# Kernel tuning notes

Hardware: AMD Instinct MI355X
Metric: run time of the kernel (lower is better)

## Reference

```python
import jax, jax.numpy as jnp
import numpy as np

R = 32  # voxel resolution
B, CIN, COUT, N = 4, 64, 64, 4096
K = 3


def setup_inputs():
    key = jax.random.key(0)
    ks = jax.random.split(key, 8)
    s = 0.05
    return {
        "features": jax.random.normal(ks[0], (B, CIN, N), jnp.float32),
        "coords": jax.random.normal(ks[1], (B, 3, N), jnp.float32),
        # voxel branch: conv3d + BN x2
        "w1": jax.random.normal(ks[2], (COUT, CIN, K, K, K), jnp.float32) * s,
        "b1": jnp.zeros((COUT,), jnp.float32),
        "g1": jnp.ones((COUT,), jnp.float32),
        "be1": jnp.zeros((COUT,), jnp.float32),
        "w2": jax.random.normal(ks[3], (COUT, COUT, K, K, K), jnp.float32) * s,
        "b2": jnp.zeros((COUT,), jnp.float32),
        "g2": jnp.ones((COUT,), jnp.float32),
        "be2": jnp.zeros((COUT,), jnp.float32),
        # point branch SharedMLP (1x1 conv + BN + ReLU)
        "wp": jax.random.normal(ks[4], (COUT, CIN), jnp.float32) * s,
        "bp": jnp.zeros((COUT,), jnp.float32),
        "gp": jnp.ones((COUT,), jnp.float32),
        "bep": jnp.zeros((COUT,), jnp.float32),
        # fuzzy_proj 1x1 conv
        "wf": jax.random.normal(ks[5], (COUT, CIN), jnp.float32) * s,
        "bf": jnp.zeros((COUT,), jnp.float32),
        # fusion SharedMLP (3*COUT -> COUT)
        "wfu": jax.random.normal(ks[6], (COUT, 3 * COUT), jnp.float32) * s,
        "bfu": jnp.zeros((COUT,), jnp.float32),
        "gfu": jnp.ones((COUT,), jnp.float32),
        "befu": jnp.zeros((COUT,), jnp.float32),
    }


def _bn3d(x, g, b):
    # training-mode BatchNorm3d, eps=1e-4 (biased variance, as torch)
    m = x.mean((0, 2, 3, 4), keepdims=True)
    v = x.var((0, 2, 3, 4), keepdims=True)
    return (x - m) * jax.lax.rsqrt(v + 1e-4) * g[None, :, None, None, None] + b[None, :, None, None, None]


def _bn1d(x, g, b):
    m = x.mean((0, 2), keepdims=True)
    v = x.var((0, 2), keepdims=True)
    return (x - m) * jax.lax.rsqrt(v + 1e-4) * g[None, :, None] + b[None, :, None]


def _conv3d(x, w, b):
    pad = K // 2
    y = jax.lax.conv_general_dilated(x, w, (1, 1, 1), [(pad, pad)] * 3,
                                     dimension_numbers=('NCDHW', 'OIDHW', 'NCDHW'))
    return y + b[None, :, None, None, None]


def _conv1x1(x, w, b):
    return jnp.einsum('oc,bcn->bon', w, x) + b[None, :, None]


def _voxelize(features, coords):
    # PVCNN Voxelization(normalize=True, eps=0): center, scale to unit, grid coords in [0, R-1]
    nc = coords - coords.mean(axis=2, keepdims=True)              # [B,3,N]
    norm = jnp.linalg.norm(nc, axis=1, keepdims=True)             # [B,1,N]
    nc = nc / (norm.max(axis=2, keepdims=True) * 2.0) + 0.5
    nc = jnp.clip(nc * R, 0.0, R - 1)
    vox = jnp.round(nc).astype(jnp.int32)                         # [B,3,N]
    b_, c_, n_ = features.shape
    idx = (vox[:, 0] * R + vox[:, 1]) * R + vox[:, 2]             # [B,N]
    flat = (idx + jnp.arange(b_)[:, None] * R ** 3).reshape(-1)
    feat = features.transpose(0, 2, 1).reshape(b_ * n_, c_)
    sums = jax.ops.segment_sum(feat, flat, num_segments=b_ * R ** 3)
    cnt = jax.ops.segment_sum(jnp.ones((b_ * n_,), feat.dtype), flat, num_segments=b_ * R ** 3)
    avg = sums / jnp.maximum(cnt, 1.0)[:, None]                   # scatter-mean
    grid = avg.reshape(b_, R ** 3, c_).transpose(0, 2, 1).reshape(b_, c_, R, R, R)
    return grid, nc


def _devoxelize(grid, nc):
    # trilinear gather: grid [B,C,R,R,R], nc [B,3,N] float coords in [0,R-1]
    b_, c_ = grid.shape[:2]
    g = grid.reshape(b_, c_, -1)
    lo_f = jnp.floor(nc)
    fr = nc - lo_f                                                # fractional part [B,3,N]
    lo = lo_f.astype(jnp.int32)
    hi = jnp.minimum(lo + 1, R - 1)
    out = jnp.zeros((b_, c_, nc.shape[2]), grid.dtype)
    for dx in (0, 1):
        for dy in (0, 1):
            for dz in (0, 1):
                ix = hi[:, 0] if dx else lo[:, 0]
                iy = hi[:, 1] if dy else lo[:, 1]
                iz = hi[:, 2] if dz else lo[:, 2]
                w = ((fr[:, 0] if dx else 1.0 - fr[:, 0]) *
                     (fr[:, 1] if dy else 1.0 - fr[:, 1]) *
                     (fr[:, 2] if dz else 1.0 - fr[:, 2]))        # [B,N]
                flat = (ix * R + iy) * R + iz                     # [B,N]
                vals = jnp.take_along_axis(g, flat[:, None, :], axis=2)  # [B,C,N]
                out = out + vals * w[:, None, :]
    return out


def reference(features, coords, w1, b1, g1, be1, w2, b2, g2, be2,
              wp, bp, gp, bep, wf, bf, wfu, bfu, gfu, befu):
    lrelu = lambda x: jnp.where(x > 0, x, 0.1 * x)
    # voxel branch
    grid, nc = _voxelize(features, coords)
    v = lrelu(_bn3d(_conv3d(grid, w1, b1), g1, be1))
    v = lrelu(_bn3d(_conv3d(v, w2, b2), g2, be2))
    vox_feat = _devoxelize(v, nc)                                 # [B,COUT,N]
    # point branch
    pt = jax.nn.relu(_bn1d(_conv1x1(features, wp, bp), gp, bep))
    # fuzzy branch: dense attention over points
    cn = coords.transpose(0, 2, 1)                                # [B,N,3]
    cn = cn / jnp.maximum(jnp.linalg.norm(cn, axis=-1, keepdims=True), 1e-12)
    att = jax.nn.softmax(jnp.einsum('bnd,bmd->bnm', cn, cn) / 0.1, axis=-1)
    fz = jnp.einsum('bnm,bcm->bcn', att, features)                # [B,CIN,N]
    fz = _conv1x1(fz, wf, bf)
    # fusion
    comb = jnp.concatenate([vox_feat, pt, fz], axis=1)            # [B,3*COUT,N]
    fused = jax.nn.relu(_bn1d(_conv1x1(comb, wfu, bfu), gfu, befu))
    return (fused, coords)
```

## Files before the change

kernel.cpp:

```cpp
#include <hip/hip_runtime.h>
#include <hip/hip_bf16.h>
#include <math.h>

#define RR 32
#define R3 32768
#define BB 4
#define CI 64
#define CO 64
#define NN 4096

typedef short v8s __attribute__((ext_vector_type(8)));
typedef float v4f __attribute__((ext_vector_type(4)));
typedef unsigned short ushort_t;

__device__ __forceinline__ unsigned short f2bf(float f) {
    unsigned int u = __float_as_uint(f);
    unsigned int r = (u + 0x7FFFu + ((u >> 16) & 1u)) >> 16;
    return (unsigned short)r;
}
__device__ __forceinline__ float bf2f(unsigned short h) {
    return __uint_as_float((unsigned int)h << 16);
}

__device__ __forceinline__ void gll16(const void* g, void* l) {
    __builtin_amdgcn_global_load_lds((const __attribute__((address_space(1))) unsigned int*)g,
                                     (__attribute__((address_space(3))) unsigned int*)l, 16, 0, 0);
}

__device__ __forceinline__ float blockReduceSum(float v, float* sm) {
    int tid = threadIdx.x;
    sm[tid] = v; __syncthreads();
    for (int off = 128; off > 0; off >>= 1) {
        if (tid < off) sm[tid] += sm[tid + off];
        __syncthreads();
    }
    float r = sm[0]; __syncthreads();
    return r;
}
__device__ __forceinline__ float blockReduceMax(float v, float* sm) {
    int tid = threadIdx.x;
    sm[tid] = v; __syncthreads();
    for (int off = 128; off > 0; off >>= 1) {
        if (tid < off) sm[tid] = fmaxf(sm[tid], sm[tid + off]);
        __syncthreads();
    }
    float r = sm[0]; __syncthreads();
    return r;
}

__global__ void k_nc(const float* __restrict__ coords, float* __restrict__ nc,
                     int* __restrict__ vidx, int* __restrict__ cntI) {
    int b = blockIdx.x, tid = threadIdx.x;
    __shared__ float sm[256];
    const float* cb = coords + (size_t)b * 3 * NN;
    float s0 = 0, s1 = 0, s2 = 0;
    for (int n = tid; n < NN; n += 256) {
        s0 += cb[n]; s1 += cb[NN + n]; s2 += cb[2 * NN + n];
    }
    float m0 = blockReduceSum(s0, sm) * (1.0f / NN);
    float m1 = blockReduceSum(s1, sm) * (1.0f / NN);
    float m2 = blockReduceSum(s2, sm) * (1.0f / NN);
    float mx = 0;
    for (int n = tid; n < NN; n += 256) {
        float dx = cb[n] - m0, dy = cb[NN + n] - m1, dz = cb[2 * NN + n] - m2;
        mx = fmaxf(mx, dx * dx + dy * dy + dz * dz);
    }
    mx = blockReduceMax(mx, sm);
    float denom = 2.0f * sqrtf(mx);
    float mean[3] = {m0, m1, m2};
    for (int n = tid; n < NN; n += 256) {
        int vi[3];
        #pragma unroll
        for (int ax = 0; ax < 3; ax++) {
            float x = (cb[ax * NN + n] - mean[ax]) / denom + 0.5f;
            x = x * RR;
            x = fminf(fmaxf(x, 0.0f), (float)(RR - 1));
            nc[((size_t)b * 3 + ax) * NN + n] = x;
            vi[ax] = (int)rintf(x);
        }
        int idx = (vi[0] * RR + vi[1]) * RR + vi[2];
        vidx[b * NN + n] = idx;
        atomicAdd(&cntI[b * R3 + idx], 1);
    }
}

__global__ void k_scan1(const int* __restrict__ cntI, int* __restrict__ lscan,
                        int* __restrict__ bsum) {
    __shared__ int sm[256];
    int tid = threadIdx.x;
    int i = blockIdx.x * 256 + tid;
    int v = cntI[i];
    sm[tid] = v; __syncthreads();
    for (int off = 1; off < 256; off <<= 1) {
        int t = (tid >= off) ? sm[tid - off] : 0;
        __syncthreads();
        sm[tid] += t;
        __syncthreads();
    }
    lscan[i] = sm[tid] - v;
    if (tid == 255) bsum[blockIdx.x] = sm[tid];
}

__global__ void k_scan2(const int* __restrict__ bsum, int* __restrict__ bbase) {
    __shared__ int sm[512];
    int tid = threadIdx.x;
    int v = bsum[tid];
    sm[tid] = v; __syncthreads();
    for (int off = 1; off < 512; off <<= 1) {
        int t = (tid >= off) ? sm[tid - off] : 0;
        __syncthreads();
        sm[tid] += t;
        __syncthreads();
    }
    bbase[tid] = sm[tid] - v;
}

__global__ void k_fill(const int* __restrict__ vidx, const int* __restrict__ lscan,
                       const int* __restrict__ bbase, int* __restrict__ rank,
                       int* __restrict__ plist) {
    int i = blockIdx.x * 256 + threadIdx.x;
    int b = i >> 12, n = i & (NN - 1);
    int flat = b * R3 + vidx[i];
    int r = atomicAdd(&rank[flat], 1);
    plist[bbase[flat >> 8] + lscan[flat] + r] = n;
}

__global__ void k_pfeat(const float* __restrict__ feat, float* __restrict__ featT,
                        ushort_t* __restrict__ featb) {
    __shared__ float t[64][65];
    int b = blockIdx.y, n0 = blockIdx.x * 64, tid = threadIdx.x;
    int q = tid >> 6, nl = tid & 63;
    #pragma unroll
    for (int k = 0; k < 16; k++) {
        int c = q * 16 + k;
        float v = feat[((size_t)(b * CI + c)) * NN + n0 + nl];
        t[nl][c] = v;
        featb[((size_t)(b * CI + c)) * NN + n0 + nl] = f2bf(v);
    }
    __syncthreads();
    #pragma unroll
    for (int k = 0; k < 16; k++) {
        int n = q * 16 + k;
        featT[((size_t)b * NN + n0 + n) * 64 + nl] = t[n][nl];
    }
}

__global__ __launch_bounds__(256) void k_gather(const float* __restrict__ featT,
                                                const int* __restrict__ cntI,
                                                const int* __restrict__ lscan,
                                                const int* __restrict__ bbase,
                                                const int* __restrict__ plist,
                                                ushort_t* __restrict__ gT) {
    int wv = threadIdx.x >> 6, lane = threadIdx.x & 63;
    int vbase = blockIdx.x * 32 + wv * 8;
    for (int k = 0; k < 8; k++) {
        int flat = vbase + k;
        int count = cntI[flat];
        float s = 0.0f;
        if (count > 0) {
            int b = flat >> 15;
            int start = bbase[flat >> 8] + lscan[flat];
            for (int j = 0; j < count; j++) {
                int n = plist[start + j];
                s += featT[((size_t)b * NN + n) * 64 + lane];
            }
            s *= 1.0f / (float)count;
        }
        gT[(size_t)flat * 64 + lane] = f2bf(s);
    }
}

__global__ void k_tws(const float* __restrict__ w1, const float* __restrict__ w2,
                      ushort_t* __restrict__ wS1, ushort_t* __restrict__ wS2) {
    int i = blockIdx.x * 256 + threadIdx.x;
    const float* w = (i < 110592) ? w1 : w2;
    ushort_t* wS = (i < 110592) ? wS1 : wS2;
    int j = (i < 110592) ? i : i - 110592;
    int cis = j & 31, co = (j >> 5) & 63;
    int dx = (j >> 11) % 3, cih = (j / 6144) & 1, dzdy = j / 12288;
    int k = dzdy * 3 + dx, ci = cih * 32 + cis;
    wS[j] = f2bf(w[((size_t)co * CI + ci) * 27 + k]);
}

__global__ void k_fold(const float* __restrict__ wp, const float* __restrict__ wfu,
                       const float* __restrict__ wf, const float* __restrict__ bf,
                       const float* __restrict__ bfu,
                       float* __restrict__ wpT, float* __restrict__ wfuT,
                       float* __restrict__ bC, float* __restrict__ accs) {
    int i = blockIdx.x * 256 + threadIdx.x;
    if (i < 4096) {
        int c = i >> 6, o = i & 63;
        wpT[c * 64 + o] = wp[o * 64 + c];
    } else if (i < 12288) {
        int j = i - 4096;
        int c = j >> 6, o = j & 63;
        wfuT[c * 64 + o] = wfu[(size_t)o * 192 + c];
    } else if (i < 16384) {
        int j = i - 12288;
        int c = j >> 6, o = j & 63;
        float s = 0;
        for (int k = 0; k < 64; k++)
            s += wfu[(size_t)o * 192 + 128 + k] * wf[(size_t)k * 64 + c];
        wfuT[(128 + c) * 64 + o] = s;
    } else if (i < 16448) {
        int o = i - 16384;
        float s = bfu[o];
        for (int k = 0; k < 64; k++)
            s += wfu[(size_t)o * 192 + 128 + k] * bf[k];
        bC[o] = s;
    } else if (i < 16960) {
        accs[i - 16448] = 0.0f;
    }
}

__global__ void k_bncast2(const ushort_t* __restrict__ x, const float* __restrict__ accs,
                          const float* __restrict__ g, const float* __restrict__ be,
                          float invcnt, float slope, ushort_t* __restrict__ o) {
    size_t i = (size_t)blockIdx.x * 256 + threadIdx.x;
    int c0 = (int)((i * 8) & 63);
    float sc[8], sh[8];
    #pragma unroll
    for (int j = 0; j < 8; j++) {
        int c = c0 + j;
        float mean = accs[2 * c] * invcnt;
        float var = accs[2 * c + 1] * invcnt - mean * mean;
        float scale = g[c] * rsqrtf(var + 1e-4f);
        sc[j] = scale;
        sh[j] = be[c] - mean * scale;
    }
    uint4 in = ((const uint4*)x)[i];
    unsigned iv[4] = {in.x, in.y, in.z, in.w};
    unsigned pk[4];
    #pragma unroll
    for (int j = 0; j < 4; j++) {
        float u0 = bf2f((unsigned short)(iv[j] & 0xFFFF)) * sc[2 * j] + sh[2 * j];
        float u1 = bf2f((unsigned short)(iv[j] >> 16)) * sc[2 * j + 1] + sh[2 * j + 1];
        u0 = u0 > 0 ? u0 : slope * u0;
        u1 = u1 > 0 ? u1 : slope * u1;
        pk[j] = (unsigned)f2bf(u0) | ((unsigned)f2bf(u1) << 16);
    }
    ((uint4*)o)[i] = make_uint4(pk[0], pk[1], pk[2], pk[3]);
}

template <int OUTBF16>
__global__ __launch_bounds__(256) void k_convlds(const ushort_t* __restrict__ gT,
                                                 const ushort_t* __restrict__ wS,
                                                 void* __restrict__ outP,
                                                 float* __restrict__ accs) {
    __shared__ ushort_t lin[20480];
    __shared__ ushort_t lw[2][6144];
    int bid = blockIdx.x;
    int wgid = (bid & 7) * 64 + (bid >> 3);
    int yt = wgid & 3, z0 = (wgid >> 2) & 31, b = wgid >> 7;
    int tid = threadIdx.x;
    int w = __builtin_amdgcn_readfirstlane(tid >> 6);
    int lane = tid & 63, l15 = lane & 15, l4 = lane >> 4;
    int y0 = yt * 8;
    const ushort_t* gTb = gT + (size_t)b * R3 * 64;

    int voxF[4];
    #pragma unroll
    for (int f = 0; f < 4; f++)
        voxF[f] = (w * 2 + (f >> 1)) * 32 + (f & 1) * 16 + l15 - 1;
    bool xlo_ok = (l15 != 0), xhi_ok = (l15 != 15);

    int lsw = lane ^ ((lane >> 3) & 7);
    int wsz8 = ((l15 * 4 + l4) ^ ((l15 >> 1) & 7)) * 8;

    const v8s vzero = {};
    v4f acc[4][4];
    #pragma unroll
    for (int m = 0; m < 4; m++)
        #pragma unroll
        for (int f = 0; f < 4; f++)
            acc[m][f] = (v4f){0.0f, 0.0f, 0.0f, 0.0f};

#define WSTAGE(s)                                                              \
    do {                                                                       \
        const ushort_t* _src = wS + (size_t)(s) * 6144;                        \
        ushort_t* _dst = lw[(s) & 1];                                          \
        _Pragma("unroll") for (int _i = 0; _i < 3; _i++) {                     \
            int _pb = _i * 256 + w * 64;                                       \
            gll16(_src + (size_t)(_pb + lsw) * 8, _dst + (size_t)(_pb + lane) * 8); \
        }                                                                      \
    } while (0)

#define ISTAGE(dz)                                                             \
    do {                                                                       \
        int _zp = z0 - 1 + (dz);                                               \
        if (_zp < 0 || _zp > 31) {                                             \
            for (int _q = 0; _q < 10; _q++)                                    \
                *(v8s*)&lin[(size_t)(w * 640 + _q * 64 + lane) * 8] = vzero;   \
        } else {                                                               \
            if (yt == 0) *(v8s*)&lin[(size_t)tid * 8] = vzero;                 \
            if (yt == 3) *(v8s*)&lin[(size_t)(2304 + tid) * 8] = vzero;        \
            const ushort_t* _pb = gTb + ((size_t)_zp * 1024 + (size_t)(y0 - 1) * 32) * 64; \
            int _g0 = (yt == 0) ? 256 : 0;                                     \
            int _nc = 10 - (yt == 0) - (yt == 3);                              \
            for (int _i = 0; _i < _nc; _i++) {                                 \
                int _pbase = _g0 + _i * 256 + w * 64;                          \
                int _p = _pbase + lane;                                        \
                int _vx = _p >> 3, _js = _p & 7;                               \
                int _sg = _vx * 8 + (_js ^ (_vx & 7));                         \
                gll16(_pb + (size_t)_sg * 8, lin + (size_t)_pbase * 8);        \
            }                                                                  \
        }                                                                      \
    } while (0)

    WSTAGE(0);
    for (int s = 0; s < 18; s++) {
        int dy = (s / 2) % 3, cih = s & 1;
        asm volatile("s_barrier" ::: "memory");
        if ((s % 6) == 0) ISTAGE(s / 6);
        if (s + 1 < 18) WSTAGE(s + 1);
        if (s + 1 < 18) asm volatile("s_waitcnt vmcnt(3) lgkmcnt(0)" ::: "memory");
        else            asm volatile("s_waitcnt vmcnt(0) lgkmcnt(0)" ::: "memory");
        asm volatile("s_barrier" ::: "memory");

        const ushort_t* lwb = lw[s & 1];
        #pragma unroll
        for (int dx = 0; dx < 3; dx++) {
            v8s Bf[4];
            #pragma unroll
            for (int f = 0; f < 4; f++) {
                int vox = voxF[f] + dy * 32 + dx;
                int g = vox * 8 + ((cih * 4 + l4) ^ (vox & 7));
                int bix = g * 16;
                bix = bix < 0 ? 0 : bix;
                v8s vb = *(const v8s*)((const char*)lin + bix);
                bool ok = (dx == 0 && (f & 1) == 0) ? xlo_ok :
                          (dx == 2 && (f & 1) == 1) ? xhi_ok : true;
                Bf[f] = ok ? vb : vzero;
            }
            const ushort_t* ap = lwb + dx * 2048 + wsz8;
            #pragma unroll
            for (int m = 0; m < 4; m++) {
                v8s Af = *(const v8s*)(ap + m * 512);
                #pragma unroll
                for (int f = 0; f < 4; f++)
                    acc[m][f] = __builtin_amdgcn_mfma_f32_16x16x32_bf16(Af, Bf[f], acc[m][f], 0, 0, 0);
            }
        }
    }

    #pragma unroll
    for (int m = 0; m < 4; m++) {
        #pragma unroll
        for (int f = 0; f < 4; f++) {
            int y = y0 + w * 2 + (f >> 1);
            int x = (f & 1) * 16 + l15;
            size_t base = ((size_t)b * R3 + z0 * 1024 + y * 32 + x) * 64 + m * 16 + l4 * 4;
            if (OUTBF16) {
                unsigned p0 = (unsigned)f2bf(acc[m][f][0]) | ((unsigned)f2bf(acc[m][f][1]) << 16);
                unsigned p1 = (unsigned)f2bf(acc[m][f][2]) | ((unsigned)f2bf(acc[m][f][3]) << 16);
                *(uint2*)&((ushort_t*)outP)[base] = make_uint2(p0, p1);
            } else {
                float4 o = make_float4(acc[m][f][0], acc[m][f][1], acc[m][f][2], acc[m][f][3]);
                *(float4*)&((float*)outP)[base] = o;
            }
        }
    }

    __syncthreads();
    float* sbuf = (float*)lin;
    #pragma unroll
    for (int m = 0; m < 4; m++)
        #pragma unroll
        for (int r = 0; r < 4; r++) {
            float s = 0, q = 0;
            #pragma unroll
            for (int f = 0; f < 4; f++) {
                float v = acc[m][f][r];
                s += v; q += v * v;
            }
            sbuf[tid * 33 + (m * 4 + r) * 2] = s;
            sbuf[tid * 33 + (m * 4 + r) * 2 + 1] = q;
        }
    __syncthreads();
    if (tid < 128) {
        int co = tid >> 1, val = tid & 1;
        int m = co >> 4, cl4 = (co >> 2) & 3, r = co & 3;
        float a = 0;
        for (int w2 = 0; w2 < 4; w2++)
            for (int l = 0; l < 16; l++)
                a += sbuf[(w2 * 64 + cl4 * 16 + l) * 33 + (m * 4 + r) * 2 + val];
        atomicAdd(&accs[2 * co + val], a);
    }
#undef WSTAGE
#undef ISTAGE
}

__global__ void k_bnfin2(const float* __restrict__ pst, const float* __restrict__ g,
                         const float* __restrict__ be, float* __restrict__ stats,
                         float invcnt) {
    int c = blockIdx.x, tid = threadIdx.x;
    __shared__ float rs[256], rq[256];
    rs[tid] = pst[(c * 256 + tid) * 2];
    rq[tid] = pst[(c * 256 + tid) * 2 + 1];
    __syncthreads();
    for (int off = 128; off > 0; off >>= 1) {
        if (tid < off) { rs[tid] += rs[tid + off]; rq[tid] += rq[tid + off]; }
        __syncthreads();
    }
    if (tid == 0) {
        float mean = rs[0] * invcnt;
        float var = rq[0] * invcnt - mean * mean;
        float sc = g[c] * rsqrtf(var + 1e-4f);
        stats[2 * c] = sc;
        stats[2 * c + 1] = be[c] - mean * sc;
    }
}

__global__ void k_bn_act(const float* __restrict__ x, const float* __restrict__ stats,
                         float* __restrict__ out, int shift, float slope) {
    size_t i = (size_t)blockIdx.x * 256 + threadIdx.x;
    int c = (int)((i >> shift) & 63);
    float sc = stats[2 * c], sh = stats[2 * c + 1];
    float4 v = ((const float4*)x)[i];
    v.x = v.x * sc + sh; v.y = v.y * sc + sh; v.z = v.z * sc + sh; v.w = v.w * sc + sh;
    v.x = v.x > 0 ? v.x : slope * v.x;
    v.y = v.y > 0 ? v.y : slope * v.y;
    v.z = v.z > 0 ? v.z : slope * v.z;
    v.w = v.w > 0 ? v.w : slope * v.w;
    ((float4*)out)[i] = v;
}

__global__ void k_devox2(const ushort_t* __restrict__ gcl, const float* __restrict__ accs,
                         const float* __restrict__ g, const float* __restrict__ be,
                         float invcnt, const float* __restrict__ nc,
                         float* __restrict__ out) {
    int b = blockIdx.y;
    int tid = threadIdx.x, p = tid >> 4, q = tid & 15;
    int n = blockIdx.x * 16 + p;
    float x = nc[((size_t)b * 3 + 0) * NN + n];
    float y = nc[((size_t)b * 3 + 1) * NN + n];
    float z = nc[((size_t)b * 3 + 2) * NN + n];
    float fx = floorf(x), fy = floorf(y), fz = floorf(z);
    int lx = (int)fx, ly = (int)fy, lz = (int)fz;
    int hx = min(lx + 1, RR - 1), hy = min(ly + 1, RR - 1), hz = min(lz + 1, RR - 1);
    float frx = x - fx, fry = y - fy, frz = z - fz;
    int xx[2] = {lx, hx}, yy[2] = {ly, hy}, zz[2] = {lz, hz};
    float wx[2] = {1.0f - frx, frx}, wy[2] = {1.0f - fry, fry}, wz[2] = {1.0f - frz, frz};
    float sc[4], sh[4];
    #pragma unroll
    for (int j = 0; j < 4; j++) {
        int c = q * 4 + j;
        float mean = accs[2 * c] * invcnt;
        float var = accs[2 * c + 1] * invcnt - mean * mean;
        float scale = g[c] * rsqrtf(var + 1e-4f);
        sc[j] = scale;
        sh[j] = be[c] - mean * scale;
    }
    float a0 = 0, a1 = 0, a2 = 0, a3 = 0;
    #pragma unroll
    for (int dx = 0; dx < 2; dx++)
        #pragma unroll
        for (int dy = 0; dy < 2; dy++)
            #pragma unroll
            for (int dz = 0; dz < 2; dz++) {
                int idx = (xx[dx] * RR + yy[dy]) * RR + zz[dz];
                float wt = wx[dx] * wy[dy] * wz[dz];
                uint2 pv = *(const uint2*)&gcl[((size_t)b * R3 + idx) * 64 + q * 4];
                float v0 = bf2f((unsigned short)(pv.x & 0xFFFF));
                float v1 = bf2f((unsigned short)(pv.x >> 16));
                float v2 = bf2f((unsigned short)(pv.y & 0xFFFF));
                float v3 = bf2f((unsigned short)(pv.y >> 16));
                float u0 = v0 * sc[0] + sh[0]; u0 = u0 > 0 ? u0 : 0.1f * u0;
                float u1 = v1 * sc[1] + sh[1]; u1 = u1 > 0 ? u1 : 0.1f * u1;
                float u2 = v2 * sc[2] + sh[2]; u2 = u2 > 0 ? u2 : 0.1f * u2;
                float u3 = v3 * sc[3] + sh[3]; u3 = u3 > 0 ? u3 : 0.1f * u3;
                a0 += wt * u0; a1 += wt * u1; a2 += wt * u2; a3 += wt * u3;
            }
    out[((size_t)(b * 64 + q * 4 + 0)) * NN + n] = a0;
    out[((size_t)(b * 64 + q * 4 + 1)) * NN + n] = a1;
    out[((size_t)(b * 64 + q * 4 + 2)) * NN + n] = a2;
    out[((size_t)(b * 64 + q * 4 + 3)) * NN + n] = a3;
}

__global__ __launch_bounds__(256) void k_fuzzym(const float* __restrict__ coords,
                                                const ushort_t* __restrict__ featb,
                                                float* __restrict__ pnum,
                                                float* __restrict__ pden) {
    __shared__ float cm[3][1024];
    __shared__ ushort_t la[4][2048];
    int b = blockIdx.z, mc = blockIdx.y, nt = blockIdx.x;
    int tid = threadIdx.x;
    int w = tid >> 6, lane = tid & 63, l15 = lane & 15, l4 = lane >> 4;
    int m0 = mc * 1024;

    for (int i = tid; i < 1024; i += 256) {
        float a0 = coords[((size_t)b * 3 + 0) * NN + m0 + i];
        float a1 = coords[((size_t)b * 3 + 1) * NN + m0 + i];
        float a2 = coords[((size_t)b * 3 + 2) * NN + m0 + i];
        float inv = 1.0f / fmaxf(sqrtf(a0 * a0 + a1 * a1 + a2 * a2), 1e-12f);
        cm[0][i] = a0 * inv; cm[1][i] = a1 * inv; cm[2][i] = a2 * inv;
    }

    int n = nt * 64 + w * 16 + l15;
    float q0 = coords[((size_t)b * 3 + 0) * NN + n];
    float q1 = coords[((size_t)b * 3 + 1) * NN + n];
    float q2 = coords[((size_t)b * 3 + 2) * NN + n];
    float qi = 10.0f / fmaxf(sqrtf(q0 * q0 + q1 * q1 + q2 * q2), 1e-12f);
    q0 *= qi; q1 *= qi; q2 *= qi;

    int srow = tid >> 2, sslot = tid & 3;
    int g0 = sslot ^ ((srow >> 1) & 3);
    const ushort_t* fb = featb + (size_t)b * 64 * NN + m0;
    const ushort_t* sbase = fb + (size_t)srow * NN + g0 * 8;
    int rsw = (l15 >> 1) & 3;

    v4f acc[4];
    #pragma unroll
    for (int cb = 0; cb < 4; cb++) acc[cb] = (v4f){0.0f, 0.0f, 0.0f, 0.0f};
    float den = 0.0f;

    gll16(sbase, &la[0][(size_t)tid * 8]);
    gll16(sbase + 32, &la[1][(size_t)tid * 8]);
    gll16(sbase + 64, &la[2][(size_t)tid * 8]);
    __syncthreads();

    for (int t = 0; t < 32; t++) {
        int cur = t & 3;
        asm volatile("s_waitcnt vmcnt(2)" ::: "memory");
        __syncthreads();
        if (t + 3 < 32)
            gll16(sbase + (t + 3) * 32, &la[(t + 3) & 3][(size_t)tid * 8]);

        int mo = t * 32 + l4 * 8;
        float e[8];
        #pragma unroll
        for (int jj = 0; jj < 2; jj++) {
            float4 x0 = *(const float4*)&cm[0][mo + jj * 4];
            float4 x1 = *(const float4*)&cm[1][mo + jj * 4];
            float4 x2 = *(const float4*)&cm[2][mo + jj * 4];
            e[jj * 4 + 0] = __expf(q0 * x0.x + q1 * x1.x + q2 * x2.x);
            e[jj * 4 + 1] = __expf(q0 * x0.y + q1 * x1.y + q2 * x2.y);
            e[jj * 4 + 2] = __expf(q0 * x0.z + q1 * x1.z + q2 * x2.z);
            e[jj * 4 + 3] = __expf(q0 * x0.w + q1 * x1.w + q2 * x2.w);
        }
        den += ((e[0] + e[1]) + (e[2] + e[3])) + ((e[4] + e[5]) + (e[6] + e[7]));
        union { __hip_bfloat162 h[4]; v8s v; } pk;
        pk.h[0] = __float22bfloat162_rn(make_float2(e[0], e[1]));
        pk.h[1] = __float22bfloat162_rn(make_float2(e[2], e[3]));
        pk.h[2] = __float22bfloat162_rn(make_float2(e[4], e[5]));
        pk.h[3] = __float22bfloat162_rn(make_float2(e[6], e[7]));
        #pragma unroll
        for (int cb = 0; cb < 4; cb++) {
            v8s A = *(const v8s*)&la[cur][(size_t)((cb * 16 + l15) * 4 + (l4 ^ rsw)) * 8];
            acc[cb] = __builtin_amdgcn_mfma_f32_16x16x32_bf16(A, pk.v, acc[cb], 0, 0, 0);
        }
        __syncthreads();
    }

    den += __shfl_xor(den, 16);
    den += __shfl_xor(den, 32);

    size_t obase = ((size_t)(b * 4 + mc)) * 64 * NN;
    #pragma unroll
    for (int cb = 0; cb < 4; cb++)
        #pragma unroll
        for (int r = 0; r < 4; r++)
            pnum[obase + (size_t)(cb * 16 + l4 * 4 + r) * NN + n] = acc[cb][r];
    if (l4 == 0) pden[((size_t)(b * 4 + mc)) * NN + n] = den;
}

__global__ void k_combine2(const float* __restrict__ pnum, const float* __restrict__ pden,
                           float* __restrict__ fzf) {
    int i = blockIdx.x * 256 + threadIdx.x;
    int b = i >> 18, c = (i >> 12) & 63, n = i & 4095;
    float num = 0, den = 0;
    #pragma unroll
    for (int ch = 0; ch < 4; ch++) {
        num += pnum[((size_t)(b * 4 + ch) * 64 + c) * NN + n];
        den += pden[((size_t)(b * 4 + ch)) * NN + n];
    }
    fzf[((size_t)(b * 64 + c)) * NN + n] = num / den;
}

__global__ __launch_bounds__(256) void k_1x1s(const float* __restrict__ in,
                                              const float* __restrict__ wT,
                                              const float* __restrict__ bias,
                                              float* __restrict__ out,
                                              float* __restrict__ pst) {
    int b = blockIdx.z, ob = blockIdx.y, bx = blockIdx.x;
    int tid = threadIdx.x;
    int q = tid & 15, o = ob * 16 + (tid >> 4);
    int n = bx * 64 + q * 4;
    const float* src = in + (size_t)b * 64 * NN + n;
    const float* wp_ = wT + o;
    v4f acc = {0, 0, 0, 0};
    #pragma unroll 8
    for (int c = 0; c < 64; c++) {
        float4 x = *(const float4*)&src[(size_t)c * NN];
        float w = wp_[c * 64];
        acc[0] += x.x * w; acc[1] += x.y * w; acc[2] += x.z * w; acc[3] += x.w * w;
    }
    float bv = bias[o];
    float s = 0, q2 = 0;
    float4 ov;
    float* op = (float*)&ov;
    #pragma unroll
    for (int v = 0; v < 4; v++) {
        float val = acc[v] + bv;
        op[v] = val;
        s += val; q2 += val * val;
    }
    *(float4*)&out[((size_t)(b * 64 + o)) * NN + n] = ov;
    #pragma unroll
    for (int off = 1; off < 16; off <<= 1) {
        s += __shfl_xor(s, off);
        q2 += __shfl_xor(q2, off);
    }
    if (q == 0) {
        int part = bx * 4 + b;
        pst[(o * 256 + part) * 2] = s;
        pst[(o * 256 + part) * 2 + 1] = q2;
    }
}

__global__ __launch_bounds__(256) void k_1x1f(const float* __restrict__ vox,
                                              const float* __restrict__ pt,
                                              const float* __restrict__ fzf,
                                              const float* __restrict__ bnB,
                                              const float* __restrict__ wfuT,
                                              const float* __restrict__ bC,
                                              float* __restrict__ out,
                                              float* __restrict__ pst) {
    int b = blockIdx.z, ob = blockIdx.y, bx = blockIdx.x;
    int tid = threadIdx.x;
    int q = tid & 15, o = ob * 16 + (tid >> 4);
    int n = bx * 64 + q * 4;
    const float* srcA = vox + (size_t)b * 64 * NN + n;
    const float* srcB = pt + (size_t)b * 64 * NN + n;
    const float* srcC = fzf + (size_t)b * 64 * NN + n;
    const float* wA = wfuT + o;
    v4f acc = {0, 0, 0, 0};
    #pragma unroll 8
    for (int c = 0; c < 64; c++) {
        float4 x = *(const float4*)&srcA[(size_t)c * NN];
        float w = wA[c * 64];
        acc[0] += x.x * w; acc[1] += x.y * w; acc[2] += x.z * w; acc[3] += x.w * w;
    }
    #pragma unroll 8
    for (int c = 0; c < 64; c++) {
        float4 x = *(const float4*)&srcB[(size_t)c * NN];
        float sc = bnB[2 * c], sh = bnB[2 * c + 1];
        float w = wA[(64 + c) * 64];
        float x0 = fmaxf(x.x * sc + sh, 0.0f), x1 = fmaxf(x.y * sc + sh, 0.0f);
        float x2 = fmaxf(x.z * sc + sh, 0.0f), x3 = fmaxf(x.w * sc + sh, 0.0f);
        acc[0] += x0 * w; acc[1] += x1 * w; acc[2] += x2 * w; acc[3] += x3 * w;
    }
    #pragma unroll 8
    for (int c = 0; c < 64; c++) {
        float4 x = *(const float4*)&srcC[(size_t)c * NN];
        float w = wA[(128 + c) * 64];
        acc[0] += x.x * w; acc[1] += x.y * w; acc[2] += x.z * w; acc[3] += x.w * w;
    }
    float bv = bC[o];
    float s = 0, q2 = 0;
    float4 ov;
    float* op = (float*)&ov;
    #pragma unroll
    for (int v = 0; v < 4; v++) {
        float val = acc[v] + bv;
        op[v] = val;
        s += val; q2 += val * val;
    }
    *(float4*)&out[((size_t)(b * 64 + o)) * NN + n] = ov;
    #pragma unroll
    for (int off = 1; off < 16; off <<= 1) {
        s += __shfl_xor(s, off);
        q2 += __shfl_xor(q2, off);
    }
    if (q == 0) {
        int part = bx * 4 + b;
        pst[(o * 256 + part) * 2] = s;
        pst[(o * 256 + part) * 2 + 1] = q2;
    }
}

extern "C" void kernel_launch(void* const* d_in, const int* in_sizes, int n_in,
                              void* d_out, int out_size, void* d_ws, size_t ws_size,
                              hipStream_t stream) {
    const float* features = (const float*)d_in[0];
    const float* coords = (const float*)d_in[1];
    const float* w1 = (const float*)d_in[2];
    const float* g1 = (const float*)d_in[4];
    const float* be1 = (const float*)d_in[5];
    const float* w2 = (const float*)d_in[6];
    const float* g2 = (const float*)d_in[8];
    const float* be2 = (const float*)d_in[9];
    const float* wp = (const float*)d_in[10];
    const float* bp = (const float*)d_in[11];
    const float* gp = (const float*)d_in[12];
    const float* bep = (const float*)d_in[13];
    const float* wf = (const float*)d_in[14];
    const float* bf = (const float*)d_in[15];
    const float* wfu = (const float*)d_in[16];
    const float* bfu = (const float*)d_in[17];
    const float* gfu = (const float*)d_in[18];
    const float* befu = (const float*)d_in[19];

    float* ws = (float*)d_ws;
    float* nc = ws;
    int* vidx = (int*)(ws + 49152);
    int* cntI = (int*)(ws + 65536);
    float* pden = ws + 65536;
    float* gridCL = ws + 196608;
    ushort_t* gTraw = (ushort_t*)gridCL;
    int* rank = (int*)(ws + 196608);
    int* lscan = (int*)(ws + 327680);
    int* bsum = (int*)(ws + 458752);
    int* bbase = (int*)(ws + 459264);
    int* plist = (int*)(ws + 459776);
    float* featT = ws + 476160;
    float* gTpool = ws + 8585216;
    ushort_t* gT = (ushort_t*)gTpool;
    float* pnum = gTpool;
    float* pstB = gTpool + 4194304;
    float* stats = ws + 16973824;
    float* voxreg = ws + 16974336;
    ushort_t* wS1 = (ushort_t*)voxreg;
    ushort_t* wS2 = wS1 + 110592;
    float* vox = voxreg;
    float* pt = ws + 18022912;
    float* fzf = ws + 19071488;
    float* wpT = ws + 20120064;
    float* wfuT = wpT + 4096;
    float* bC = wfuT + 12288;
    float* fpre = ws + 21168640;
    ushort_t* featb = (ushort_t*)fpre;
    float* accs = ws + 22217216;

    float* out = (float*)d_out;

    hipMemsetAsync(cntI, 0, (size_t)131072 * 4, stream);
    hipMemsetAsync(rank, 0, (size_t)131072 * 4, stream);

    k_fold<<<67, 256, 0, stream>>>(wp, wfu, wf, bf, bfu, wpT, wfuT, bC, accs);
    k_pfeat<<<dim3(64, BB), 256, 0, stream>>>(features, featT, featb);
    k_tws<<<864, 256, 0, stream>>>(w1, w2, wS1, wS2);

    k_nc<<<BB, 256, 0, stream>>>(coords, nc, vidx, cntI);
    k_scan1<<<512, 256, 0, stream>>>(cntI, lscan, bsum);
    k_scan2<<<1, 512, 0, stream>>>(bsum, bbase);
    k_fill<<<BB * NN / 256, 256, 0, stream>>>(vidx, lscan, bbase, rank, plist);
    k_gather<<<4096, 256, 0, stream>>>(featT, cntI, lscan, bbase, plist, gT);

    k_convlds<1><<<512, 256, 0, stream>>>(gT, wS1, gTraw, accs);
    k_bncast2<<<BB * R3 * 64 / 8 / 256, 256, 0, stream>>>(gTraw, accs, g1, be1,
                                                          1.0f / (BB * R3), 0.1f, gT);
    k_convlds<1><<<512, 256, 0, stream>>>(gT, wS2, gTraw, accs + 128);
    k_devox2<<<dim3(NN / 16, BB), 256, 0, stream>>>(gTraw, accs + 128, g2, be2,
                                                    1.0f / (BB * R3), nc, vox);

    k_fuzzym<<<dim3(64, 4, BB), 256, 0, stream>>>(coords, featb, pnum, pden);
    k_combine2<<<BB * 64 * NN / 256, 256, 0, stream>>>(pnum, pden, fzf);

    k_1x1s<<<dim3(NN / 64, 4, BB), 256, 0, stream>>>(features, wpT, bp, pt, pstB);
    k_bnfin2<<<64, 256, 0, stream>>>(pstB, gp, bep, stats + 256, 1.0f / (BB * NN));

    k_1x1f<<<dim3(NN / 64, 4, BB), 256, 0, stream>>>(vox, pt, fzf, stats + 256, wfuT, bC,
                                                     fpre, pstB);
    k_bnfin2<<<64, 256, 0, stream>>>(pstB, gfu, befu, stats + 384, 1.0f / (BB * NN));
    k_bn_act<<<BB * 64 * NN / 4 / 256, 256, 0, stream>>>(fpre, stats + 384, out, 10, 0.0f);

    hipMemcpyAsync(out + (size_t)BB * CO * NN, coords, (size_t)BB * 3 * NN * 4,
                   hipMemcpyDeviceToDevice, stream);
}
```

Before: 269.5 us.

## Merge prep kernels, fold memsets and BN finalize, drop fuzzy-loop barriers

Three preprocessing kernels (weight fold, weight swizzle, feature transpose) and the cntI memset become one block-indexed k_prep launch. The rank memset moves into k_scan1, and the final BN-statistics kernel is merged into the BN+ReLU kernel, which redoes the per-channel reduction in every block. The combine kernel is vectorised to float4. The __syncthreads in the k_fuzzym LDS pipeline are removed. The aim is fewer launches and less fixed per-kernel overhead, but dropping those barriers risks LDS races in the multi-buffered loop.

```diff
diff --git a/kernel.cpp b/kernel.cpp
--- a/kernel.cpp
+++ b/kernel.cpp
@@ -46,6 +46,74 @@
     }
     float r = sm[0]; __syncthreads();
     return r;
+}
+
+__global__ void k_prep(const float* __restrict__ wp, const float* __restrict__ wfu,
+                       const float* __restrict__ wf, const float* __restrict__ bf,
+                       const float* __restrict__ bfu,
+                       float* __restrict__ wpT, float* __restrict__ wfuT,
+                       float* __restrict__ bC, float* __restrict__ accs,
+                       const float* __restrict__ w1, const float* __restrict__ w2,
+                       ushort_t* __restrict__ wS1, ushort_t* __restrict__ wS2,
+                       const float* __restrict__ feat, float* __restrict__ featT,
+                       ushort_t* __restrict__ featb, int* __restrict__ cntI) {
+    __shared__ float t[64][65];
+    int bid = blockIdx.x, tid = threadIdx.x;
+    if (bid < 67) {
+        int i = bid * 256 + tid;
+        if (i < 4096) {
+            int c = i >> 6, o = i & 63;
+            wpT[c * 64 + o] = wp[o * 64 + c];
+        } else if (i < 12288) {
+            int j = i - 4096;
+            int c = j >> 6, o = j & 63;
+            wfuT[c * 64 + o] = wfu[(size_t)o * 192 + c];
+        } else if (i < 16384) {
+            int j = i - 12288;
+            int c = j >> 6, o = j & 63;
+            float s = 0;
+            for (int k = 0; k < 64; k++)
+                s += wfu[(size_t)o * 192 + 128 + k] * wf[(size_t)k * 64 + c];
+            wfuT[(128 + c) * 64 + o] = s;
+        } else if (i < 16448) {
+            int o = i - 16384;
+            float s = bfu[o];
+            for (int k = 0; k < 64; k++)
+                s += wfu[(size_t)o * 192 + 128 + k] * bf[k];
+            bC[o] = s;
+        } else if (i < 16960) {
+            accs[i - 16448] = 0.0f;
+        }
+    } else if (bid < 931) {
+        int i = (bid - 67) * 256 + tid;
+        const float* w = (i < 110592) ? w1 : w2;
+        ushort_t* wS = (i < 110592) ? wS1 : wS2;
+        int j = (i < 110592) ? i : i - 110592;
+        int cis = j & 31, co = (j >> 5) & 63;
+        int dx = (j >> 11) % 3, cih = (j / 6144) & 1, dzdy = j / 12288;
+        int k = dzdy * 3 + dx, ci = cih * 32 + cis;
+        wS[j] = f2bf(w[((size_t)co * CI + ci) * 27 + k]);
+    } else if (bid < 1187) {
+        int pb = bid - 931;
+        int b = pb >> 6, n0 = (pb & 63) * 64;
+        int q = tid >> 6, nl = tid & 63;
+        #pragma unroll
+        for (int k = 0; k < 16; k++) {
+            int c = q * 16 + k;
+            float v = feat[((size_t)(b * CI + c)) * NN + n0 + nl];
+            t[nl][c] = v;
+            featb[((size_t)(b * CI + c)) * NN + n0 + nl] = f2bf(v);
+        }
+        __syncthreads();
+        #pragma unroll
+        for (int k = 0; k < 16; k++) {
+            int n = q * 16 + k;
+            featT[((size_t)b * NN + n0 + n) * 64 + nl] = t[n][nl];
+        }
+    } else {
+        int z = (bid - 1187) * 256 + tid;
+        cntI[z] = 0;
+    }
 }
 
 __global__ void k_nc(const float* __restrict__ coords, float* __restrict__ nc,
@@ -85,10 +153,11 @@
 }
 
 __global__ void k_scan1(const int* __restrict__ cntI, int* __restrict__ lscan,
-                        int* __restrict__ bsum) {
+                        int* __restrict__ bsum, int* __restrict__ rank) {
     __shared__ int sm[256];
     int tid = threadIdx.x;
     int i = blockIdx.x * 256 + tid;
+    rank[i] = 0;
     int v = cntI[i];
     sm[tid] = v; __syncthreads();
     for (int off = 1; off < 256; off <<= 1) {
@@ -123,26 +192,6 @@
     int flat = b * R3 + vidx[i];
     int r = atomicAdd(&rank[flat], 1);
     plist[bbase[flat >> 8] + lscan[flat] + r] = n;
-}
-
-__global__ void k_pfeat(const float* __restrict__ feat, float* __restrict__ featT,
-                        ushort_t* __restrict__ featb) {
-    __shared__ float t[64][65];
-    int b = blockIdx.y, n0 = blockIdx.x * 64, tid = threadIdx.x;
-    int q = tid >> 6, nl = tid & 63;
-    #pragma unroll
-    for (int k = 0; k < 16; k++) {
-        int c = q * 16 + k;
-        float v = feat[((size_t)(b * CI + c)) * NN + n0 + nl];
-        t[nl][c] = v;
-        featb[((size_t)(b * CI + c)) * NN + n0 + nl] = f2bf(v);
-    }
-    __syncthreads();
-    #pragma unroll
-    for (int k = 0; k < 16; k++) {
-        int n = q * 16 + k;
-        featT[((size_t)b * NN + n0 + n) * 64 + nl] = t[n][nl];
-    }
 }
 
 __global__ __launch_bounds__(256) void k_gather(const float* __restrict__ featT,
@@ -167,49 +216,6 @@
             s *= 1.0f / (float)count;
         }
         gT[(size_t)flat * 64 + lane] = f2bf(s);
-    }
-}
-
-__global__ void k_tws(const float* __restrict__ w1, const float* __restrict__ w2,
-                      ushort_t* __restrict__ wS1, ushort_t* __restrict__ wS2) {
-    int i = blockIdx.x * 256 + threadIdx.x;
-    const float* w = (i < 110592) ? w1 : w2;
-    ushort_t* wS = (i < 110592) ? wS1 : wS2;
-    int j = (i < 110592) ? i : i - 110592;
-    int cis = j & 31, co = (j >> 5) & 63;
-    int dx = (j >> 11) % 3, cih = (j / 6144) & 1, dzdy = j / 12288;
-    int k = dzdy * 3 + dx, ci = cih * 32 + cis;
-    wS[j] = f2bf(w[((size_t)co * CI + ci) * 27 + k]);
-}
-
-__global__ void k_fold(const float* __restrict__ wp, const float* __restrict__ wfu,
-                       const float* __restrict__ wf, const float* __restrict__ bf,
-                       const float* __restrict__ bfu,
-                       float* __restrict__ wpT, float* __restrict__ wfuT,
-                       float* __restrict__ bC, float* __restrict__ accs) {
-    int i = blockIdx.x * 256 + threadIdx.x;
-    if (i < 4096) {
-        int c = i >> 6, o = i & 63;
-        wpT[c * 64 + o] = wp[o * 64 + c];
-    } else if (i < 12288) {
-        int j = i - 4096;
-        int c = j >> 6, o = j & 63;
-        wfuT[c * 64 + o] = wfu[(size_t)o * 192 + c];
-    } else if (i < 16384) {
-        int j = i - 12288;
-        int c = j >> 6, o = j & 63;
-        float s = 0;
-        for (int k = 0; k < 64; k++)
-            s += wfu[(size_t)o * 192 + 128 + k] * wf[(size_t)k * 64 + c];
-        wfuT[(128 + c) * 64 + o] = s;
-    } else if (i < 16448) {
-        int o = i - 16384;
-        float s = bfu[o];
-        for (int k = 0; k < 64; k++)
-            s += wfu[(size_t)o * 192 + 128 + k] * bf[k];
-        bC[o] = s;
-    } else if (i < 16960) {
-        accs[i - 16448] = 0.0f;
     }
 }
 
@@ -411,17 +417,35 @@
     }
 }
 
-__global__ void k_bn_act(const float* __restrict__ x, const float* __restrict__ stats,
-                         float* __restrict__ out, int shift, float slope) {
-    size_t i = (size_t)blockIdx.x * 256 + threadIdx.x;
-    int c = (int)((i >> shift) & 63);
-    float sc = stats[2 * c], sh = stats[2 * c + 1];
+__global__ void k_bnact2(const float* __restrict__ x, const float* __restrict__ pst,
+                         const float* __restrict__ g, const float* __restrict__ be,
+                         float invcnt, float* __restrict__ out) {
+    int bid = blockIdx.x, tid = threadIdx.x;
+    int c = (bid >> 2) & 63;
+    __shared__ float rs[256], rq[256];
+    __shared__ float sscale, sshift;
+    rs[tid] = pst[(c * 256 + tid) * 2];
+    rq[tid] = pst[(c * 256 + tid) * 2 + 1];
+    __syncthreads();
+    for (int off = 128; off > 0; off >>= 1) {
+        if (tid < off) { rs[tid] += rs[tid + off]; rq[tid] += rq[tid + off]; }
+        __syncthreads();
+    }
+    if (tid == 0) {
+        float mean = rs[0] * invcnt;
+        float var = rq[0] * invcnt - mean * mean;
+        float sc = g[c] * rsqrtf(var + 1e-4f);
+        sscale = sc;
+        sshift = be[c] - mean * sc;
+    }
+    __syncthreads();
+    float sc = sscale, sh = sshift;
+    size_t i = (size_t)bid * 256 + tid;
     float4 v = ((const float4*)x)[i];
-    v.x = v.x * sc + sh; v.y = v.y * sc + sh; v.z = v.z * sc + sh; v.w = v.w * sc + sh;
-    v.x = v.x > 0 ? v.x : slope * v.x;
-    v.y = v.y > 0 ? v.y : slope * v.y;
-    v.z = v.z > 0 ? v.z : slope * v.z;
-    v.w = v.w > 0 ? v.w : slope * v.w;
+    v.x = fmaxf(v.x * sc + sh, 0.0f);
+    v.y = fmaxf(v.y * sc + sh, 0.0f);
+    v.z = fmaxf(v.z * sc + sh, 0.0f);
+    v.w = fmaxf(v.w * sc + sh, 0.0f);
     ((float4*)out)[i] = v;
 }
 
@@ -517,7 +541,6 @@
     gll16(sbase, &la[0][(size_t)tid * 8]);
     gll16(sbase + 32, &la[1][(size_t)tid * 8]);
     gll16(sbase + 64, &la[2][(size_t)tid * 8]);
-    __syncthreads();
 
     for (int t = 0; t < 32; t++) {
         int cur = t & 3;
@@ -549,7 +572,6 @@
             v8s A = *(const v8s*)&la[cur][(size_t)((cb * 16 + l15) * 4 + (l4 ^ rsw)) * 8];
             acc[cb] = __builtin_amdgcn_mfma_f32_16x16x32_bf16(A, pk.v, acc[cb], 0, 0, 0);
         }
-        __syncthreads();
     }
 
     den += __shfl_xor(den, 16);
@@ -566,15 +588,18 @@
 
 __global__ void k_combine2(const float* __restrict__ pnum, const float* __restrict__ pden,
                            float* __restrict__ fzf) {
-    int i = blockIdx.x * 256 + threadIdx.x;
-    int b = i >> 18, c = (i >> 12) & 63, n = i & 4095;
-    float num = 0, den = 0;
+    int i4 = blockIdx.x * 256 + threadIdx.x;
+    int b = i4 >> 16, c = (i4 >> 10) & 63, n4 = i4 & 1023;
+    float4 num = make_float4(0, 0, 0, 0), den = make_float4(0, 0, 0, 0);
     #pragma unroll
     for (int ch = 0; ch < 4; ch++) {
-        num += pnum[((size_t)(b * 4 + ch) * 64 + c) * NN + n];
-        den += pden[((size_t)(b * 4 + ch)) * NN + n];
-    }
-    fzf[((size_t)(b * 64 + c)) * NN + n] = num / den;
+        float4 pn = ((const float4*)pnum)[((size_t)(b * 4 + ch) * 64 + c) * 1024 + n4];
+        float4 pd = ((const float4*)pden)[(size_t)(b * 4 + ch) * 1024 + n4];
+        num.x += pn.x; num.y += pn.y; num.z += pn.z; num.w += pn.w;
+        den.x += pd.x; den.y += pd.y; den.z += pd.z; den.w += pd.w;
+    }
+    float4 o = make_float4(num.x / den.x, num.y / den.y, num.z / den.z, num.w / den.w);
+    ((float4*)fzf)[((size_t)(b * 64 + c)) * 1024 + n4] = o;
 }
 
 __global__ __launch_bounds__(256) void k_1x1s(const float* __restrict__ in,
@@ -734,15 +759,11 @@
 
     float* out = (float*)d_out;
 
-    hipMemsetAsync(cntI, 0, (size_t)131072 * 4, stream);
-    hipMemsetAsync(rank, 0, (size_t)131072 * 4, stream);
-
-    k_fold<<<67, 256, 0, stream>>>(wp, wfu, wf, bf, bfu, wpT, wfuT, bC, accs);
-    k_pfeat<<<dim3(64, BB), 256, 0, stream>>>(features, featT, featb);
-    k_tws<<<864, 256, 0, stream>>>(w1, w2, wS1, wS2);
+    k_prep<<<1699, 256, 0, stream>>>(wp, wfu, wf, bf, bfu, wpT, wfuT, bC, accs,
+                                     w1, w2, wS1, wS2, features, featT, featb, cntI);
 
     k_nc<<<BB, 256, 0, stream>>>(coords, nc, vidx, cntI);
-    k_scan1<<<512, 256, 0, stream>>>(cntI, lscan, bsum);
+    k_scan1<<<512, 256, 0, stream>>>(cntI, lscan, bsum, rank);
     k_scan2<<<1, 512, 0, stream>>>(bsum, bbase);
     k_fill<<<BB * NN / 256, 256, 0, stream>>>(vidx, lscan, bbase, rank, plist);
     k_gather<<<4096, 256, 0, stream>>>(featT, cntI, lscan, bbase, plist, gT);
@@ -755,15 +776,15 @@
                                                     1.0f / (BB * R3), nc, vox);
 
     k_fuzzym<<<dim3(64, 4, BB), 256, 0, stream>>>(coords, featb, pnum, pden);
-    k_combine2<<<BB * 64 * NN / 256, 256, 0, stream>>>(pnum, pden, fzf);
+    k_combine2<<<BB * 64 * NN / 4 / 256, 256, 0, stream>>>(pnum, pden, fzf);
 
     k_1x1s<<<dim3(NN / 64, 4, BB), 256, 0, stream>>>(features, wpT, bp, pt, pstB);
     k_bnfin2<<<64, 256, 0, stream>>>(pstB, gp, bep, stats + 256, 1.0f / (BB * NN));
 
     k_1x1f<<<dim3(NN / 64, 4, BB), 256, 0, stream>>>(vox, pt, fzf, stats + 256, wfuT, bC,
                                                      fpre, pstB);
-    k_bnfin2<<<64, 256, 0, stream>>>(pstB, gfu, befu, stats + 384, 1.0f / (BB * NN));
-    k_bn_act<<<BB * 64 * NN / 4 / 256, 256, 0, stream>>>(fpre, stats + 384, out, 10, 0.0f);
+    k_bnact2<<<BB * 64 * NN / 4 / 256, 256, 0, stream>>>(fpre, pstB, gfu, befu,
+                                                         1.0f / (BB * NN), out);
 
     hipMemcpyAsync(out + (size_t)BB * CO * NN, coords, (size_t)BB * 3 * NN * 4,
                    hipMemcpyDeviceToDevice, stream);
```

Result: faster. 256.6 us (-4.8%).
